# Kernel optimization log

Measured on AMD Instinct MI355X. Metric: run time of the kernel, lower is better.

The kernel has to match this reference:

```python
import jax, jax.numpy as jnp
import numpy as np

IN_FEATURES = 512
OUT_FEATURES = 128
KERNEL_DIM = 32
BATCH = 128


def setup_inputs() -> dict:
    key = jax.random.key(0)
    kx, kT = jax.random.split(key)
    x = jax.random.normal(kx, (BATCH, IN_FEATURES), dtype=jnp.float32)
    # nn.Parameter initialized with normal(0, 1)
    T = jax.random.normal(kT, (IN_FEATURES, OUT_FEATURES, KERNEL_DIM), dtype=jnp.float32)
    return {"x": x, "T": T}


def reference(x, T):
    B = x.shape[0]
    in_f, out_f, k_dim = T.shape
    # projection: [B, in] @ [in, out*k] -> [B, out, k]
    m = (x @ T.reshape(in_f, out_f * k_dim)).reshape(B, out_f, k_dim)
    # pairwise L1 distance over kernel dim: [B, B, out]
    # original: M = m[None], M_T = m[:, None]; norm = |M - M_T|.sum(3); o_b = exp(-norm).sum(0) - 1
    norm = jnp.abs(m[None, :, :, :] - m[:, None, :, :]).sum(axis=-1)  # [i=B, j=B, out]
    o_b = jnp.exp(-norm).sum(axis=0) - 1.0  # [B, out] (subtract self-distance term exp(0)=1)
    return jnp.concatenate([x, o_b], axis=1)  # [B, in + out]
```

## Files before the change

### kernel.cpp

```cpp
#include <hip/hip_runtime.h>
#include <hip/hip_fp16.h>

#define IN_F    512
#define NC      4096
#define OUT_COLS 640
#define B_SZ    128
#define MOH_PITCH 72

typedef __attribute__((ext_vector_type(8))) short  bf16x8;
typedef __attribute__((ext_vector_type(4))) float  f32x4;

union H2x4 { uint4 u4; __half2 h[4]; };

static __device__ __forceinline__ unsigned short f2bfu(float f) {
    return (unsigned short)(__float_as_uint(f) >> 16);
}
static __device__ __forceinline__ unsigned int pack2(float lo, float hi) {
    return (__float_as_uint(lo) >> 16) | (__float_as_uint(hi) & 0xFFFF0000u);
}
static __device__ __forceinline__ __half2 habs2_(__half2 v) {
    unsigned int u = *(unsigned int*)&v & 0x7FFF7FFFu;
    return *(__half2*)&u;
}

__global__ __launch_bounds__(256) void prep_kernel(
    const float* __restrict__ x, float* __restrict__ out,
    unsigned short* __restrict__ xa)
{
    const int g = blockIdx.x * 256 + threadIdx.x;
    const int b = g >> 7, c4 = g & 127;
    float4 v = ((const float4*)x)[g];
    *(float4*)(out + b * OUT_COLS + c4 * 4) = v;
    const int slot = ((b >> 4) * 16 + (c4 >> 3)) * 64 + ((c4 >> 1) & 3) * 16 + (b & 15);
    uint2 pv; pv.x = pack2(v.x, v.y); pv.y = pack2(v.z, v.w);
    *(uint2*)(xa + (size_t)slot * 8 + (c4 & 1) * 4) = pv;
}

__global__ __launch_bounds__(1024) void fused_kernel(
    const unsigned short* __restrict__ xa,
    const float* __restrict__ T,
    float* __restrict__ out)
{
    __shared__ unsigned short bs[2 * 16 * 64 * 8];
    __shared__ __align__(16) __half moh[B_SZ * MOH_PITCH];
    __shared__ float psum[2 * 32 * 33];

    const int tid   = threadIdx.x;
    const int lane  = tid & 63;
    const int w     = tid >> 6;
    const int col   = lane & 15;
    const int q     = lane >> 4;
    const int o     = blockIdx.x >> 1;
    const int jhalf = blockIdx.x & 1;
    const int mt    = w >> 1, nt = w & 1;

    #pragma unroll
    for (int p = 0; p < 4; ++p) {
        int u  = tid + p * 1024;
        int kk = u >> 3, cq = u & 7;
        float4 v = *(const float4*)(T + (size_t)kk * NC + o * 32 + cq * 4);
        int kt = kk >> 5, qq = (kk >> 3) & 3, j = kk & 7;
        float e[4] = {v.x, v.y, v.z, v.w};
        #pragma unroll
        for (int r = 0; r < 4; ++r) {
            int nn = cq * 4 + r;
            int slot = (((nn >> 4) * 16 + kt) * 64) + qq * 16 + (nn & 15);
            bs[slot * 8 + j] = f2bfu(e[r]);
        }
    }
    __syncthreads();

    f32x4 acc = {0.f, 0.f, 0.f, 0.f};
    const unsigned short* pa = xa + ((size_t)(mt * 16) * 64 + lane) * 8;
    const unsigned short* pb = bs + ((size_t)(nt * 16) * 64 + lane) * 8;
    #pragma unroll 4
    for (int kt = 0; kt < 16; ++kt) {
        bf16x8 af  = *(const bf16x8*)(pa + (size_t)kt * 512);
        bf16x8 bfr = *(const bf16x8*)(pb + (size_t)kt * 512);
        acc = __builtin_amdgcn_mfma_f32_16x16x32_bf16(af, bfr, acc, 0, 0, 0);
    }
    {
        const int rowb = mt * 16 + q * 4;
        #pragma unroll
        for (int r = 0; r < 4; ++r)
            moh[(rowb + r) * MOH_PITCH + nt * 16 + col] = __float2half(acc[r]);
    }
    __syncthreads();

    const int jj5 = tid & 31;
    const int isl = tid >> 5;
    const int j0  = jhalf * 64 + jj5;

    __half2 mj0[16], mj1[16];
    #pragma unroll
    for (int k16 = 0; k16 < 4; ++k16) {
        H2x4 a, b;
        a.u4 = *(const uint4*)&moh[j0 * MOH_PITCH + k16 * 8];
        b.u4 = *(const uint4*)&moh[(j0 + 32) * MOH_PITCH + k16 * 8];
        #pragma unroll
        for (int h = 0; h < 4; ++h) { mj0[k16*4+h] = a.h[h]; mj1[k16*4+h] = b.h[h]; }
    }

    float s0 = 0.f, s1 = 0.f;
    #pragma unroll
    for (int ii = 0; ii < 4; ++ii) {
        const int i = isl * 4 + ii;
        __half2 n0 = __float2half2_rn(0.f), n1 = __float2half2_rn(0.f);
        #pragma unroll
        for (int k16 = 0; k16 < 4; ++k16) {
            H2x4 mi; mi.u4 = *(const uint4*)&moh[i * MOH_PITCH + k16 * 8];
            #pragma unroll
            for (int h = 0; h < 4; ++h) {
                n0 = __hadd2(n0, habs2_(__hsub2(mj0[k16*4+h], mi.h[h])));
                n1 = __hadd2(n1, habs2_(__hsub2(mj1[k16*4+h], mi.h[h])));
            }
        }
        float2 f0 = __half22float2(n0), f1 = __half22float2(n1);
        s0 += __expf(-(f0.x + f0.y));
        s1 += __expf(-(f1.x + f1.y));
    }
    psum[jj5 * 33 + isl]        = s0;
    psum[1056 + jj5 * 33 + isl] = s1;
    __syncthreads();
    if (tid < 64) {
        int jsel = tid >> 5, jj = tid & 31;
        float tot = 0.f;
        #pragma unroll
        for (int u = 0; u < 32; ++u) tot += psum[jsel * 1056 + jj * 33 + u];
        out[(jhalf * 64 + jsel * 32 + jj) * OUT_COLS + IN_F + o] = tot - 1.0f;
    }
}

extern "C" void kernel_launch(void* const* d_in, const int* in_sizes, int n_in,
                              void* d_out, int out_size, void* d_ws, size_t ws_size,
                              hipStream_t stream) {
    const float* x = (const float*)d_in[0];
    const float* T = (const float*)d_in[1];
    float* out = (float*)d_out;
    unsigned short* xa = (unsigned short*)d_ws;

    prep_kernel<<<64, 256, 0, stream>>>(x, out, xa);
    fused_kernel<<<256, 1024, 0, stream>>>(xa, T, out);
}
```

Before: 71.27 us.

## Load T directly into 32x32 MFMA fragments with split-K and LDS reduction

Replaces the LDS staging of the T tile and the 16x16x32 MFMA loop with direct global loads of T into bf16 registers. These feed 32x32x16 MFMAs, with K split across four wave groups and partial sums reduced through shared memory before the fp16 conversion. The xa layout in the prep kernel changes to match the new A-fragment shape, and block-to-(o, jhalf) mapping is swapped so adjacent blocks share j-half. The goal is to cut the LDS scatter/transposition and the serial K loop. The cost is extra LDS traffic for the reduction, an additional barrier, and strided scalar global loads of T.

```diff
diff --git a/kernel.cpp b/kernel.cpp
--- a/kernel.cpp
+++ b/kernel.cpp
@@ -7,14 +7,12 @@
 #define B_SZ    128
 #define MOH_PITCH 72
 
-typedef __attribute__((ext_vector_type(8))) short  bf16x8;
-typedef __attribute__((ext_vector_type(4))) float  f32x4;
+typedef __attribute__((ext_vector_type(8)))  short bf16x8;
+typedef __attribute__((ext_vector_type(16))) float f32x16;
 
-union H2x4 { uint4 u4; __half2 h[4]; };
+union H2x4  { uint4 u4; __half2 h[4]; };
+union FragB { unsigned int u[4]; bf16x8 s; };
 
-static __device__ __forceinline__ unsigned short f2bfu(float f) {
-    return (unsigned short)(__float_as_uint(f) >> 16);
-}
 static __device__ __forceinline__ unsigned int pack2(float lo, float hi) {
     return (__float_as_uint(lo) >> 16) | (__float_as_uint(hi) & 0xFFFF0000u);
 }
@@ -31,7 +29,7 @@
     const int b = g >> 7, c4 = g & 127;
     float4 v = ((const float4*)x)[g];
     *(float4*)(out + b * OUT_COLS + c4 * 4) = v;
-    const int slot = ((b >> 4) * 16 + (c4 >> 3)) * 64 + ((c4 >> 1) & 3) * 16 + (b & 15);
+    const int slot = ((b >> 5) * 32 + (c4 >> 2)) * 64 + ((c4 >> 1) & 1) * 32 + (b & 31);
     uint2 pv; pv.x = pack2(v.x, v.y); pv.y = pack2(v.z, v.w);
     *(uint2*)(xa + (size_t)slot * 8 + (c4 & 1) * 4) = pv;
 }
@@ -41,49 +39,63 @@
     const float* __restrict__ T,
     float* __restrict__ out)
 {
-    __shared__ unsigned short bs[2 * 16 * 64 * 8];
-    __shared__ __align__(16) __half moh[B_SZ * MOH_PITCH];
-    __shared__ float psum[2 * 32 * 33];
+    __shared__ __align__(16) char smem[65536];
+    float*  red  = (float*)smem;
+    __half* moh  = (__half*)smem;
+    float*  psum = (float*)(smem + 18432);
 
-    const int tid   = threadIdx.x;
-    const int lane  = tid & 63;
-    const int w     = tid >> 6;
-    const int col   = lane & 15;
-    const int q     = lane >> 4;
-    const int o     = blockIdx.x >> 1;
-    const int jhalf = blockIdx.x & 1;
-    const int mt    = w >> 1, nt = w & 1;
+    const int tid    = threadIdx.x;
+    const int lane   = tid & 63;
+    const int w      = tid >> 6;
+    const int o      = blockIdx.x & 127;
+    const int jhalf  = blockIdx.x >> 7;
+    const int mt     = w & 3;
+    const int kg     = w >> 2;
+    const int col    = lane & 31;
+    const int half32 = lane >> 5;
 
+    f32x16 acc = {0.f,0.f,0.f,0.f,0.f,0.f,0.f,0.f,0.f,0.f,0.f,0.f,0.f,0.f,0.f,0.f};
+    const unsigned short* pa = xa + ((size_t)(mt * 32 + kg * 8) * 64 + lane) * 8;
+    const float* pb = T + (size_t)(kg * 128 + half32 * 8) * NC + o * 32 + col;
     #pragma unroll
-    for (int p = 0; p < 4; ++p) {
-        int u  = tid + p * 1024;
-        int kk = u >> 3, cq = u & 7;
-        float4 v = *(const float4*)(T + (size_t)kk * NC + o * 32 + cq * 4);
-        int kt = kk >> 5, qq = (kk >> 3) & 3, j = kk & 7;
-        float e[4] = {v.x, v.y, v.z, v.w};
+    for (int ch = 0; ch < 8; ++ch) {
+        bf16x8 af = *(const bf16x8*)(pa + (size_t)ch * 512);
+        const float* tb = pb + (size_t)ch * 16 * NC;
+        float b0 = tb[0*NC], b1 = tb[1*NC], b2 = tb[2*NC], b3 = tb[3*NC];
+        float b4 = tb[4*NC], b5 = tb[5*NC], b6 = tb[6*NC], b7 = tb[7*NC];
+        FragB bf;
+        bf.u[0] = pack2(b0, b1); bf.u[1] = pack2(b2, b3);
+        bf.u[2] = pack2(b4, b5); bf.u[3] = pack2(b6, b7);
+        acc = __builtin_amdgcn_mfma_f32_32x32x16_bf16(af, bf.s, acc, 0, 0, 0);
+    }
+    {
+        float* rd = red + kg * 4096 + mt * 1024 + col;
         #pragma unroll
-        for (int r = 0; r < 4; ++r) {
-            int nn = cq * 4 + r;
-            int slot = (((nn >> 4) * 16 + kt) * 64) + qq * 16 + (nn & 15);
-            bs[slot * 8 + j] = f2bfu(e[r]);
+        for (int r = 0; r < 16; ++r) {
+            int row = (r & 3) + 8 * (r >> 2) + 4 * half32;
+            rd[row * 32] = acc[r];
         }
     }
     __syncthreads();
 
-    f32x4 acc = {0.f, 0.f, 0.f, 0.f};
-    const unsigned short* pa = xa + ((size_t)(mt * 16) * 64 + lane) * 8;
-    const unsigned short* pb = bs + ((size_t)(nt * 16) * 64 + lane) * 8;
-    #pragma unroll 4
-    for (int kt = 0; kt < 16; ++kt) {
-        bf16x8 af  = *(const bf16x8*)(pa + (size_t)kt * 512);
-        bf16x8 bfr = *(const bf16x8*)(pb + (size_t)kt * 512);
-        acc = __builtin_amdgcn_mfma_f32_16x16x32_bf16(af, bfr, acc, 0, 0, 0);
+    float4 s;
+    {
+        const int e = tid * 4;
+        s = *(const float4*)&red[e];
+        #pragma unroll
+        for (int p = 1; p < 4; ++p) {
+            float4 v2 = *(const float4*)&red[p * 4096 + e];
+            s.x += v2.x; s.y += v2.y; s.z += v2.z; s.w += v2.w;
+        }
     }
+    __syncthreads();
     {
-        const int rowb = mt * 16 + q * 4;
-        #pragma unroll
-        for (int r = 0; r < 4; ++r)
-            moh[(rowb + r) * MOH_PITCH + nt * 16 + col] = __float2half(acc[r]);
+        const int e = tid * 4;
+        const int mtt = e >> 10, row = (e >> 5) & 31, c0 = e & 31;
+        __half2 lo = __floats2half2_rn(s.x, s.y);
+        __half2 hi = __floats2half2_rn(s.z, s.w);
+        uint2 w2; w2.x = *(unsigned int*)&lo; w2.y = *(unsigned int*)&hi;
+        *(uint2*)&moh[(mtt * 32 + row) * MOH_PITCH + c0] = w2;
     }
     __syncthreads();
 
```

Result: no change. 69.94 us (-1.9%).
